# Kernel optimization log

Measured on AMD Instinct MI355X. Metric: run time of the kernel, lower is better.

## Reference

```python
import jax, jax.numpy as jnp
import numpy as np

D = 1024
H = 16
HD = D // H


def setup_inputs() -> dict:
    key = jax.random.key(0)
    ks = jax.random.split(key, 5)
    s = 1.0 / np.sqrt(D)
    return {
        "inputs": jax.random.normal(ks[0], (2, 2048, D), dtype=jnp.float32),
        "Wq": jax.random.normal(ks[1], (D, D), dtype=jnp.float32) * s,
        "bq": jnp.zeros((D,), jnp.float32),
        "Wk": jax.random.normal(ks[2], (D, D), dtype=jnp.float32) * s,
        "bk": jnp.zeros((D,), jnp.float32),
        "Wv": jax.random.normal(ks[3], (D, D), dtype=jnp.float32) * s,
        "bv": jnp.zeros((D,), jnp.float32),
        "Wo": jax.random.normal(ks[4], (D, D), dtype=jnp.float32) * s,
        "bo": jnp.zeros((D,), jnp.float32),
    }


def reference(inputs, Wq, bq, Wk, bk, Wv, bv, Wo, bo):
    B, S, _ = inputs.shape
    def split_heads(x):  # [B,S,D] -> [B,H,S,hd]
        return x.reshape(B, S, H, HD).transpose(0, 2, 1, 3)
    q = split_heads(inputs @ Wq + bq)
    k = split_heads(inputs @ Wk + bk)
    v = split_heads(inputs @ Wv + bv)
    scale = 1.0 / jnp.sqrt(jnp.asarray(HD, inputs.dtype))
    scores = jnp.einsum("bhsd,bhtd->bhst", q, k) * scale  # [B,H,S,S]
    weights = jax.nn.softmax(scores, axis=-1)
    attn = jnp.einsum("bhst,bhtd->bhsd", weights, v)
    concat = attn.transpose(0, 2, 1, 3).reshape(B, S, D)
    return concat @ Wo + bo
```

## Files before the change

### kernel.cpp

```cpp
#include <hip/hip_runtime.h>


typedef __bf16 bf16x8 __attribute__((ext_vector_type(8)));
typedef float  f32x4  __attribute__((ext_vector_type(4)));

#if __has_builtin(__builtin_amdgcn_exp2f)
#define EXPFN(x) __builtin_amdgcn_exp2f(x)
#define QSCALE (0.125f * 1.44269504088896f)
#else
#define EXPFN(x) __expf(x)
#define QSCALE 0.125f
#endif

#define LDKP 74

__device__ __forceinline__ unsigned short f2bf(float f) {
    unsigned int u = __float_as_uint(f);
    u += 0x7FFFu + ((u >> 16) & 1u);
    return (unsigned short)(u >> 16);
}

__device__ __forceinline__ void gload16(const void* g, void* l) {
    __builtin_amdgcn_global_load_lds(
        (const __attribute__((address_space(1))) void*)g,
        (__attribute__((address_space(3))) void*)l, 16, 0, 0);
}

#define WAIT0_BARRIER() asm volatile("s_waitcnt vmcnt(0)\n\ts_barrier" ::: "memory")

__global__ __launch_bounds__(256) void prep_kernel(
    const float* __restrict__ X, ushort4* __restrict__ Xb,
    const float* __restrict__ Wq, const float* __restrict__ Wk,
    const float* __restrict__ Wv, const float* __restrict__ Wo,
    unsigned short* __restrict__ Wt_all) {
    const int z = blockIdx.z;
    if (z == 4) {
        int base = (blockIdx.y * 32 + blockIdx.x) * 1024 + threadIdx.x;
        const float4* X4 = (const float4*)X;
        #pragma unroll
        for (int c = 0; c < 4; c++) {
            int i = base + c * 256;
            float4 v = X4[i];
            ushort4 o;
            o.x = f2bf(v.x); o.y = f2bf(v.y); o.z = f2bf(v.z); o.w = f2bf(v.w);
            Xb[i] = o;
        }
        return;
    }
    __shared__ float tile[32][33];
    const float* W = (z == 0) ? Wq : (z == 1) ? Wk : (z == 2) ? Wv : Wo;
    unsigned short* Wt = Wt_all + (size_t)z * 1024 * 1024;
    int c0 = blockIdx.x * 32, r0 = blockIdx.y * 32;
    int x = threadIdx.x & 31, y = threadIdx.x >> 5;
    for (int j = 0; j < 32; j += 8)
        tile[y + j][x] = W[(r0 + y + j) * 1024 + c0 + x];
    __syncthreads();
    for (int j = 0; j < 32; j += 8)
        Wt[(c0 + y + j) * 1024 + r0 + x] = f2bf(tile[x][y + j]);
}

__global__ __launch_bounds__(256) void gemm_qkv_kernel(
    const unsigned short* __restrict__ Xb, const unsigned short* __restrict__ Wt_all,
    const float* __restrict__ bq, const float* __restrict__ bk,
    const float* __restrict__ bv,
    unsigned short* __restrict__ Qb, unsigned short* __restrict__ Kb,
    unsigned short* __restrict__ Vt) {
    const int z = blockIdx.z;
    const int x0 = blockIdx.x * 128;
    const int y0 = blockIdx.y * 128;

    const unsigned short* Ap;
    const unsigned short* Bp;
    if (z < 2) {
        Ap = Xb + (size_t)x0 * 1024;
        Bp = Wt_all + (size_t)z * 1024 * 1024 + (size_t)y0 * 1024;
    } else {
        Ap = Wt_all + (size_t)2 * 1024 * 1024 + (size_t)y0 * 1024;
        Bp = Xb + (size_t)x0 * 1024;
    }

    __shared__ __align__(16) unsigned short As[128 * 64];
    __shared__ __align__(16) unsigned short Bs[128 * 64];

    const int tid = threadIdx.x;
    const int lane = tid & 63, wave = tid >> 6;
    const int quad = lane >> 4, l15 = lane & 15;
    const int wrow = (wave >> 1) * 64, wcol = (wave & 1) * 64;

    f32x4 acc[4][4] = {};

    const int srow = lane >> 3;
    const int ch8  = (lane & 7) * 8;
    const int swz  = (((lane & 7) ^ srow)) * 8;
    const int sw   = (l15 & 7);

    for (int k0 = 0; k0 < 1024; k0 += 64) {
        #pragma unroll
        for (int c = 0; c < 4; c++) {
            int r = c * 32 + wave * 8 + srow;
            gload16(Ap + (size_t)r * 1024 + k0 + swz, &As[r * 64 + ch8]);
            gload16(Bp + (size_t)r * 1024 + k0 + swz, &Bs[r * 64 + ch8]);
        }
        WAIT0_BARRIER();
        #pragma unroll
        for (int kk = 0; kk < 2; kk++) {
            bf16x8 af[4], bfr[4];
            #pragma unroll
            for (int i = 0; i < 4; i++)
                af[i] = *(const bf16x8*)&As[(wrow + i * 16 + l15) * 64 +
                                            (((kk * 4 + quad) ^ sw)) * 8];
            #pragma unroll
            for (int j = 0; j < 4; j++)
                bfr[j] = *(const bf16x8*)&Bs[(wcol + j * 16 + l15) * 64 +
                                             (((kk * 4 + quad) ^ sw)) * 8];
            #pragma unroll
            for (int i = 0; i < 4; i++)
                #pragma unroll
                for (int j = 0; j < 4; j++)
                    acc[i][j] = __builtin_amdgcn_mfma_f32_16x16x32_bf16(
                        af[i], bfr[j], acc[i][j], 0, 0, 0);
        }
        __syncthreads();
    }

    if (z < 2) {
        const float* bias = (z == 0) ? bq : bk;
        #pragma unroll
        for (int j = 0; j < 4; j++) {
            int col = y0 + wcol + j * 16 + l15;
            float bcol = bias[col];
            int h = col >> 6, d = col & 63;
            #pragma unroll
            for (int i = 0; i < 4; i++)
                #pragma unroll
                for (int r = 0; r < 4; r++) {
                    int row = x0 + wrow + i * 16 + quad * 4 + r;
                    int b = row >> 11, s = row & 2047;
                    float v = acc[i][j][r] + bcol;
                    if (z == 0)
                        Qb[(size_t)((b * 16 + h) * 2048 + s) * 64 + d] = f2bf(v * QSCALE);
                    else
                        Kb[(size_t)((b * 16 + h) * 2048 + s) * 64 + d] = f2bf(v);
                }
        }
    } else {
        #pragma unroll
        for (int i = 0; i < 4; i++)
            #pragma unroll
            for (int r = 0; r < 4; r++) {
                int rowd = y0 + wrow + i * 16 + quad * 4 + r;
                float brow = bv[rowd];
                #pragma unroll
                for (int j = 0; j < 4; j++) {
                    int colm = x0 + wcol + j * 16 + l15;
                    int b = colm >> 11, s = colm & 2047;
                    Vt[(size_t)(b * 1024 + rowd) * 2048 + s] = f2bf(acc[i][j][r] + brow);
                }
            }
    }
}

__global__ __launch_bounds__(256) void attn_kernel(
    const unsigned short* __restrict__ Qb, const unsigned short* __restrict__ Kb,
    const unsigned short* __restrict__ Vt, unsigned short* __restrict__ Cc,
    float* __restrict__ Op, float* __restrict__ Lp, int tlen, int do_split) {
    const int bh = blockIdx.y;
    const int b = bh >> 4, h = bh & 15;
    const int q0 = blockIdx.x * 128;
    const int split = blockIdx.z;
    const int tbeg = split * tlen;

    const int tid = threadIdx.x;
    const int lane = tid & 63, wave = tid >> 6;
    const int quad = lane >> 4, l15 = lane & 15;

    __shared__ __align__(16) unsigned short Ks[2][64 * 64];
    __shared__ __align__(16) unsigned short Vs[2][64 * 64];
    __shared__ __align__(16) unsigned short Ps[4][32 * LDKP];

    const unsigned short* Qbh = Qb + (size_t)bh * 2048 * 64;
    const unsigned short* Kbh = Kb + (size_t)bh * 2048 * 64;
    const unsigned short* Vbh = Vt + (size_t)bh * 64 * 2048;

    bf16x8 qa[2][2];
    #pragma unroll
    for (int mi = 0; mi < 2; mi++)
        #pragma unroll
        for (int kk = 0; kk < 2; kk++)
            qa[mi][kk] = *(const bf16x8*)&Qbh[
                (size_t)(q0 + wave * 32 + mi * 16 + l15) * 64 + kk * 32 + quad * 8];

    union { unsigned short us[8]; bf16x8 v; } ones_u;
    #pragma unroll
    for (int i = 0; i < 8; i++) ones_u.us[i] = 0x3F80;
    const bf16x8 onesv = ones_u.v;

    f32x4 o[2][4] = {};
    f32x4 ol[2] = {};

    const int srow = lane >> 3;
    const int r0s = wave * 16 + srow;
    const int ch8 = (lane & 7) * 8;
    const int swz = (((lane & 7) ^ srow)) * 8;
    const int sw  = (l15 & 7);

    {
        const int t0 = tbeg;
        gload16(&Kbh[(size_t)(t0 + r0s) * 64 + swz],       &Ks[0][r0s * 64 + ch8]);
        gload16(&Kbh[(size_t)(t0 + r0s + 8) * 64 + swz],   &Ks[0][(r0s + 8) * 64 + ch8]);
        gload16(&Vbh[(size_t)r0s * 2048 + t0 + swz],       &Vs[0][r0s * 64 + ch8]);
        gload16(&Vbh[(size_t)(r0s + 8) * 2048 + t0 + swz], &Vs[0][(r0s + 8) * 64 + ch8]);
    }

    const int niter = tlen >> 6;
    for (int it = 0; it < niter; it++) {
        const int cur = it & 1, nxt = cur ^ 1;
        WAIT0_BARRIER();
        if (it + 1 < niter) {
            const int t0 = tbeg + (it + 1) * 64;
            gload16(&Kbh[(size_t)(t0 + r0s) * 64 + swz],       &Ks[nxt][r0s * 64 + ch8]);
            gload16(&Kbh[(size_t)(t0 + r0s + 8) * 64 + swz],   &Ks[nxt][(r0s + 8) * 64 + ch8]);
            gload16(&Vbh[(size_t)r0s * 2048 + t0 + swz],       &Vs[nxt][r0s * 64 + ch8]);
            gload16(&Vbh[(size_t)(r0s + 8) * 2048 + t0 + swz], &Vs[nxt][(r0s + 8) * 64 + ch8]);
        }

        f32x4 sf[2][4] = {};
        #pragma unroll
        for (int j = 0; j < 4; j++)
            #pragma unroll
            for (int kk = 0; kk < 2; kk++) {
                bf16x8 kf = *(const bf16x8*)&Ks[cur][(j * 16 + l15) * 64 +
                                                     (((kk * 4 + quad) ^ sw)) * 8];
                sf[0][j] = __builtin_amdgcn_mfma_f32_16x16x32_bf16(qa[0][kk], kf, sf[0][j], 0, 0, 0);
                sf[1][j] = __builtin_amdgcn_mfma_f32_16x16x32_bf16(qa[1][kk], kf, sf[1][j], 0, 0, 0);
            }

        #pragma unroll
        for (int mi = 0; mi < 2; mi++)
            #pragma unroll
            for (int j = 0; j < 4; j++)
                #pragma unroll
                for (int r = 0; r < 4; r++) {
                    float p = EXPFN(sf[mi][j][r]);
                    Ps[wave][(mi * 16 + quad * 4 + r) * LDKP + j * 16 + l15] =
                        (unsigned short)(__float_as_uint(p) >> 16);
                }

        asm volatile("s_waitcnt lgkmcnt(0)" ::: "memory");

        #pragma unroll
        for (int kk = 0; kk < 2; kk++) {
            bf16x8 pf0 = *(const bf16x8*)&Ps[wave][(l15) * LDKP + kk * 32 + quad * 8];
            bf16x8 pf1 = *(const bf16x8*)&Ps[wave][(16 + l15) * LDKP + kk * 32 + quad * 8];
            ol[0] = __builtin_amdgcn_mfma_f32_16x16x32_bf16(pf0, onesv, ol[0], 0, 0, 0);
            ol[1] = __builtin_amdgcn_mfma_f32_16x16x32_bf16(pf1, onesv, ol[1], 0, 0, 0);
            #pragma unroll
            for (int j = 0; j < 4; j++) {
                bf16x8 vf = *(const bf16x8*)&Vs[cur][(j * 16 + l15) * 64 +
                                                     (((kk * 4 + quad) ^ sw)) * 8];
                o[0][j] = __builtin_amdgcn_mfma_f32_16x16x32_bf16(pf0, vf, o[0][j], 0, 0, 0);
                o[1][j] = __builtin_amdgcn_mfma_f32_16x16x32_bf16(pf1, vf, o[1][j], 0, 0, 0);
            }
        }
    }

    if (do_split) {
        float* Opd = Op + (size_t)(split * 32 + bh) * 2048 * 64;
        float* Lpd = Lp + (size_t)(split * 32 + bh) * 2048;
        #pragma unroll
        for (int mi = 0; mi < 2; mi++)
            #pragma unroll
            for (int r = 0; r < 4; r++) {
                int s = q0 + wave * 32 + mi * 16 + quad * 4 + r;
                if (l15 == 0) Lpd[s] = ol[mi][r];
                #pragma unroll
                for (int j = 0; j < 4; j++)
                    Opd[(size_t)s * 64 + j * 16 + l15] = o[mi][j][r];
            }
    } else {
        #pragma unroll
        for (int mi = 0; mi < 2; mi++)
            #pragma unroll
            for (int r = 0; r < 4; r++) {
                float inv = 1.f / ol[mi][r];
                int s = q0 + wave * 32 + mi * 16 + quad * 4 + r;
                size_t row = (size_t)(b * 2048 + s);
                #pragma unroll
                for (int j = 0; j < 4; j++)
                    Cc[row * 1024 + h * 64 + j * 16 + l15] = f2bf(o[mi][j][r] * inv);
            }
    }
}

__global__ __launch_bounds__(256) void combine_kernel(
    const float4* __restrict__ Op, const float* __restrict__ Lp,
    unsigned short* __restrict__ Cc) {
    int idx = blockIdx.x * 256 + threadIdx.x;
    int d4 = idx & 15;
    int s = (idx >> 4) & 2047;
    int bh = idx >> 15;
    const size_t half4 = (size_t)32 * 2048 * 16;
    float4 a = Op[(size_t)idx], c = Op[half4 + (size_t)idx];
    float l = Lp[bh * 2048 + s] + Lp[32 * 2048 + bh * 2048 + s];
    float inv = 1.f / l;
    ushort4 o;
    o.x = f2bf((a.x + c.x) * inv); o.y = f2bf((a.y + c.y) * inv);
    o.z = f2bf((a.z + c.z) * inv); o.w = f2bf((a.w + c.w) * inv);
    int b = bh >> 4, h = bh & 15;
    *(ushort4*)&Cc[((size_t)(b * 2048 + s)) * 1024 + h * 64 + d4 * 4] = o;
}

__global__ __launch_bounds__(256) void gemm_out_kernel(
    const unsigned short* __restrict__ Cc, const unsigned short* __restrict__ Wot,
    const float* __restrict__ bo, float* __restrict__ out) {
    const int m0 = blockIdx.x * 128;
    const int n0 = blockIdx.y * 64;

    __shared__ __align__(16) unsigned short As[128 * 64];
    __shared__ __align__(16) unsigned short Bs[64 * 64];

    const int tid = threadIdx.x;
    const int lane = tid & 63, wave = tid >> 6;
    const int quad = lane >> 4, l15 = lane & 15;
    const int wrow = (wave >> 1) * 64, wcol = (wave & 1) * 32;

    f32x4 acc[4][2] = {};
    const int srow = lane >> 3;
    const int ch8 = (lane & 7) * 8;
    const int swz = (((lane & 7) ^ srow)) * 8;
    const int sw  = (l15 & 7);

    for (int k0 = 0; k0 < 1024; k0 += 64) {
        #pragma unroll
        for (int c = 0; c < 4; c++) {
            int r = c * 32 + wave * 8 + srow;
            gload16(Cc + (size_t)(m0 + r) * 1024 + k0 + swz, &As[r * 64 + ch8]);
            if (c < 2)
                gload16(Wot + (size_t)(n0 + r) * 1024 + k0 + swz, &Bs[r * 64 + ch8]);
        }
        WAIT0_BARRIER();
        #pragma unroll
        for (int kk = 0; kk < 2; kk++) {
            bf16x8 af[4], bfr[2];
            #pragma unroll
            for (int i = 0; i < 4; i++)
                af[i] = *(const bf16x8*)&As[(wrow + i * 16 + l15) * 64 +
                                            (((kk * 4 + quad) ^ sw)) * 8];
            #pragma unroll
            for (int j = 0; j < 2; j++)
                bfr[j] = *(const bf16x8*)&Bs[(wcol + j * 16 + l15) * 64 +
                                             (((kk * 4 + quad) ^ sw)) * 8];
            #pragma unroll
            for (int i = 0; i < 4; i++)
                #pragma unroll
                for (int j = 0; j < 2; j++)
                    acc[i][j] = __builtin_amdgcn_mfma_f32_16x16x32_bf16(
                        af[i], bfr[j], acc[i][j], 0, 0, 0);
        }
        __syncthreads();
    }

    #pragma unroll
    for (int j = 0; j < 2; j++) {
        int col = n0 + wcol + j * 16 + l15;
        float bcol = bo[col];
        #pragma unroll
        for (int i = 0; i < 4; i++)
            #pragma unroll
            for (int r = 0; r < 4; r++) {
                int row = m0 + wrow + i * 16 + quad * 4 + r;
                out[(size_t)row * 1024 + col] = acc[i][j][r] + bcol;
            }
    }
}

extern "C" void kernel_launch(void* const* d_in, const int* in_sizes, int n_in,
                              void* d_out, int out_size, void* d_ws, size_t ws_size,
                              hipStream_t stream) {
    const float* X  = (const float*)d_in[0];
    const float* Wq = (const float*)d_in[1];
    const float* bq = (const float*)d_in[2];
    const float* Wk = (const float*)d_in[3];
    const float* bk = (const float*)d_in[4];
    const float* Wv = (const float*)d_in[5];
    const float* bv = (const float*)d_in[6];
    const float* Wo = (const float*)d_in[7];
    const float* bo = (const float*)d_in[8];
    float* out = (float*)d_out;

    char* ws = (char*)d_ws;
    unsigned short* Xb = (unsigned short*)(ws);
    unsigned short* Wt = (unsigned short*)(ws + (8u  << 20));
    unsigned short* Qb = (unsigned short*)(ws + (16u << 20));
    unsigned short* Kb = (unsigned short*)(ws + (24u << 20));
    unsigned short* Vt = (unsigned short*)(ws + (32u << 20));
    unsigned short* Cc = (unsigned short*)(ws + (40u << 20));
    float* Op = (float*)(ws + (48u << 20));
    float* Lp = (float*)(ws + (48u << 20) + 33554432u);
    const bool use_split = ws_size >= ((size_t)(48u << 20) + 33554432u + 524288u);

    prep_kernel<<<dim3(32, 32, 5), 256, 0, stream>>>(X, (ushort4*)Xb, Wq, Wk, Wv, Wo, Wt);
    gemm_qkv_kernel<<<dim3(32, 8, 3), 256, 0, stream>>>(Xb, Wt, bq, bk, bv, Qb, Kb, Vt);
    if (use_split) {
        attn_kernel<<<dim3(16, 32, 2), 256, 0, stream>>>(Qb, Kb, Vt, Cc, Op, Lp, 1024, 1);
        combine_kernel<<<4096, 256, 0, stream>>>((const float4*)Op, Lp, Cc);
    } else {
        attn_kernel<<<dim3(16, 32, 1), 256, 0, stream>>>(Qb, Kb, Vt, Cc, Op, Lp, 2048, 0);
    }
    gemm_out_kernel<<<dim3(32, 16), 256, 0, stream>>>(Cc, Wt + 3u * 1024 * 1024, bo, out);
}
```

Measured before the change: 208.3 us.

## Fuse Q and K projections sharing X tile; single-buffer attention K/V loads

The QKV GEMM now computes Q and K in one block, loading the X tile once and running two accumulator sets against separate Wq and Wk tiles. The grid shrinks from three z-slices to two, and launch bounds request two blocks per CU. Separately, the attention kernel drops its double-buffered K/V prefetch in favour of a single buffer that is loaded and waited on each iteration. This cuts LDS use but exposes global load latency. The doubled accumulators raise register pressure in the fused Q/K path.

```diff
diff --git a/kernel.cpp b/kernel.cpp
--- a/kernel.cpp
+++ b/kernel.cpp
@@ -59,7 +59,7 @@
         Wt[(c0 + y + j) * 1024 + r0 + x] = f2bf(tile[x][y + j]);
 }
 
-__global__ __launch_bounds__(256) void gemm_qkv_kernel(
+__global__ __launch_bounds__(256, 2) void gemm_qkv_kernel(
     const unsigned short* __restrict__ Xb, const unsigned short* __restrict__ Wt_all,
     const float* __restrict__ bq, const float* __restrict__ bk,
     const float* __restrict__ bv,
@@ -69,66 +69,68 @@
     const int x0 = blockIdx.x * 128;
     const int y0 = blockIdx.y * 128;
 
-    const unsigned short* Ap;
-    const unsigned short* Bp;
-    if (z < 2) {
-        Ap = Xb + (size_t)x0 * 1024;
-        Bp = Wt_all + (size_t)z * 1024 * 1024 + (size_t)y0 * 1024;
-    } else {
-        Ap = Wt_all + (size_t)2 * 1024 * 1024 + (size_t)y0 * 1024;
-        Bp = Xb + (size_t)x0 * 1024;
-    }
-
     __shared__ __align__(16) unsigned short As[128 * 64];
-    __shared__ __align__(16) unsigned short Bs[128 * 64];
+    __shared__ __align__(16) unsigned short Bs0[128 * 64];
+    __shared__ __align__(16) unsigned short Bs1[128 * 64];
 
     const int tid = threadIdx.x;
     const int lane = tid & 63, wave = tid >> 6;
     const int quad = lane >> 4, l15 = lane & 15;
     const int wrow = (wave >> 1) * 64, wcol = (wave & 1) * 64;
 
-    f32x4 acc[4][4] = {};
-
     const int srow = lane >> 3;
     const int ch8  = (lane & 7) * 8;
     const int swz  = (((lane & 7) ^ srow)) * 8;
     const int sw   = (l15 & 7);
 
-    for (int k0 = 0; k0 < 1024; k0 += 64) {
-        #pragma unroll
-        for (int c = 0; c < 4; c++) {
-            int r = c * 32 + wave * 8 + srow;
-            gload16(Ap + (size_t)r * 1024 + k0 + swz, &As[r * 64 + ch8]);
-            gload16(Bp + (size_t)r * 1024 + k0 + swz, &Bs[r * 64 + ch8]);
-        }
-        WAIT0_BARRIER();
-        #pragma unroll
-        for (int kk = 0; kk < 2; kk++) {
-            bf16x8 af[4], bfr[4];
-            #pragma unroll
-            for (int i = 0; i < 4; i++)
-                af[i] = *(const bf16x8*)&As[(wrow + i * 16 + l15) * 64 +
-                                            (((kk * 4 + quad) ^ sw)) * 8];
-            #pragma unroll
-            for (int j = 0; j < 4; j++)
-                bfr[j] = *(const bf16x8*)&Bs[(wcol + j * 16 + l15) * 64 +
-                                             (((kk * 4 + quad) ^ sw)) * 8];
-            #pragma unroll
-            for (int i = 0; i < 4; i++)
-                #pragma unroll
-                for (int j = 0; j < 4; j++)
-                    acc[i][j] = __builtin_amdgcn_mfma_f32_16x16x32_bf16(
-                        af[i], bfr[j], acc[i][j], 0, 0, 0);
-        }
-        __syncthreads();
-    }
-
-    if (z < 2) {
-        const float* bias = (z == 0) ? bq : bk;
+    if (z == 0) {
+        const unsigned short* Ap = Xb + (size_t)x0 * 1024;
+        const unsigned short* Bq = Wt_all + (size_t)y0 * 1024;
+        const unsigned short* Bk = Wt_all + (size_t)1024 * 1024 + (size_t)y0 * 1024;
+
+        f32x4 aq[4][4] = {};
+        f32x4 ak[4][4] = {};
+
+        for (int k0 = 0; k0 < 1024; k0 += 64) {
+            #pragma unroll
+            for (int c = 0; c < 4; c++) {
+                int r = c * 32 + wave * 8 + srow;
+                gload16(Ap + (size_t)r * 1024 + k0 + swz, &As[r * 64 + ch8]);
+                gload16(Bq + (size_t)r * 1024 + k0 + swz, &Bs0[r * 64 + ch8]);
+                gload16(Bk + (size_t)r * 1024 + k0 + swz, &Bs1[r * 64 + ch8]);
+            }
+            WAIT0_BARRIER();
+            #pragma unroll
+            for (int kk = 0; kk < 2; kk++) {
+                bf16x8 af[4], bqf[4], bkf[4];
+                #pragma unroll
+                for (int i = 0; i < 4; i++)
+                    af[i] = *(const bf16x8*)&As[(wrow + i * 16 + l15) * 64 +
+                                                (((kk * 4 + quad) ^ sw)) * 8];
+                #pragma unroll
+                for (int j = 0; j < 4; j++) {
+                    bqf[j] = *(const bf16x8*)&Bs0[(wcol + j * 16 + l15) * 64 +
+                                                  (((kk * 4 + quad) ^ sw)) * 8];
+                    bkf[j] = *(const bf16x8*)&Bs1[(wcol + j * 16 + l15) * 64 +
+                                                  (((kk * 4 + quad) ^ sw)) * 8];
+                }
+                #pragma unroll
+                for (int i = 0; i < 4; i++)
+                    #pragma unroll
+                    for (int j = 0; j < 4; j++) {
+                        aq[i][j] = __builtin_amdgcn_mfma_f32_16x16x32_bf16(
+                            af[i], bqf[j], aq[i][j], 0, 0, 0);
+                        ak[i][j] = __builtin_amdgcn_mfma_f32_16x16x32_bf16(
+                            af[i], bkf[j], ak[i][j], 0, 0, 0);
+                    }
+            }
+            __syncthreads();
+        }
+
         #pragma unroll
         for (int j = 0; j < 4; j++) {
             int col = y0 + wcol + j * 16 + l15;
-            float bcol = bias[col];
+            float bqc = bq[col], bkc = bk[col];
             int h = col >> 6, d = col & 63;
             #pragma unroll
             for (int i = 0; i < 4; i++)
@@ -136,14 +138,46 @@
                 for (int r = 0; r < 4; r++) {
                     int row = x0 + wrow + i * 16 + quad * 4 + r;
                     int b = row >> 11, s = row & 2047;
-                    float v = acc[i][j][r] + bcol;
-                    if (z == 0)
-                        Qb[(size_t)((b * 16 + h) * 2048 + s) * 64 + d] = f2bf(v * QSCALE);
-                    else
-                        Kb[(size_t)((b * 16 + h) * 2048 + s) * 64 + d] = f2bf(v);
+                    size_t idx = (size_t)((b * 16 + h) * 2048 + s) * 64 + d;
+                    Qb[idx] = f2bf((aq[i][j][r] + bqc) * QSCALE);
+                    Kb[idx] = f2bf(ak[i][j][r] + bkc);
                 }
         }
     } else {
+        const unsigned short* Ap = Wt_all + (size_t)2 * 1024 * 1024 + (size_t)y0 * 1024;
+        const unsigned short* Bp = Xb + (size_t)x0 * 1024;
+
+        f32x4 acc[4][4] = {};
+
+        for (int k0 = 0; k0 < 1024; k0 += 64) {
+            #pragma unroll
+            for (int c = 0; c < 4; c++) {
+                int r = c * 32 + wave * 8 + srow;
+                gload16(Ap + (size_t)r * 1024 + k0 + swz, &As[r * 64 + ch8]);
+                gload16(Bp + (size_t)r * 1024 + k0 + swz, &Bs0[r * 64 + ch8]);
+            }
+            WAIT0_BARRIER();
+            #pragma unroll
+            for (int kk = 0; kk < 2; kk++) {
+                bf16x8 af[4], bfr[4];
+                #pragma unroll
+                for (int i = 0; i < 4; i++)
+                    af[i] = *(const bf16x8*)&As[(wrow + i * 16 + l15) * 64 +
+                                                (((kk * 4 + quad) ^ sw)) * 8];
+                #pragma unroll
+                for (int j = 0; j < 4; j++)
+                    bfr[j] = *(const bf16x8*)&Bs0[(wcol + j * 16 + l15) * 64 +
+                                                  (((kk * 4 + quad) ^ sw)) * 8];
+                #pragma unroll
+                for (int i = 0; i < 4; i++)
+                    #pragma unroll
+                    for (int j = 0; j < 4; j++)
+                        acc[i][j] = __builtin_amdgcn_mfma_f32_16x16x32_bf16(
+                            af[i], bfr[j], acc[i][j], 0, 0, 0);
+            }
+            __syncthreads();
+        }
+
         #pragma unroll
         for (int i = 0; i < 4; i++)
             #pragma unroll
@@ -174,8 +208,8 @@
     const int lane = tid & 63, wave = tid >> 6;
     const int quad = lane >> 4, l15 = lane & 15;
 
-    __shared__ __align__(16) unsigned short Ks[2][64 * 64];
-    __shared__ __align__(16) unsigned short Vs[2][64 * 64];
+    __shared__ __align__(16) unsigned short Ks[64 * 64];
+    __shared__ __align__(16) unsigned short Vs[64 * 64];
     __shared__ __align__(16) unsigned short Ps[4][32 * LDKP];
 
     const unsigned short* Qbh = Qb + (size_t)bh * 2048 * 64;
@@ -204,33 +238,23 @@
     const int swz = (((lane & 7) ^ srow)) * 8;
     const int sw  = (l15 & 7);
 
-    {
-        const int t0 = tbeg;
-        gload16(&Kbh[(size_t)(t0 + r0s) * 64 + swz],       &Ks[0][r0s * 64 + ch8]);
-        gload16(&Kbh[(size_t)(t0 + r0s + 8) * 64 + swz],   &Ks[0][(r0s + 8) * 64 + ch8]);
-        gload16(&Vbh[(size_t)r0s * 2048 + t0 + swz],       &Vs[0][r0s * 64 + ch8]);
-        gload16(&Vbh[(size_t)(r0s + 8) * 2048 + t0 + swz], &Vs[0][(r0s + 8) * 64 + ch8]);
-    }
-
-    const int niter = tlen >> 6;
-    for (int it = 0; it < niter; it++) {
-        const int cur = it & 1, nxt = cur ^ 1;
-        WAIT0_BARRIER();
-        if (it + 1 < niter) {
-            const int t0 = tbeg + (it + 1) * 64;
-            gload16(&Kbh[(size_t)(t0 + r0s) * 64 + swz],       &Ks[nxt][r0s * 64 + ch8]);
-            gload16(&Kbh[(size_t)(t0 + r0s + 8) * 64 + swz],   &Ks[nxt][(r0s + 8) * 64 + ch8]);
-            gload16(&Vbh[(size_t)r0s * 2048 + t0 + swz],       &Vs[nxt][r0s * 64 + ch8]);
-            gload16(&Vbh[(size_t)(r0s + 8) * 2048 + t0 + swz], &Vs[nxt][(r0s + 8) * 64 + ch8]);
-        }
+    for (int ti = 0; ti < tlen; ti += 64) {
+        const int t0 = tbeg + ti;
+        __syncthreads();
+        gload16(&Kbh[(size_t)(t0 + r0s) * 64 + swz],       &Ks[r0s * 64 + ch8]);
+        gload16(&Kbh[(size_t)(t0 + r0s + 8) * 64 + swz],   &Ks[(r0s + 8) * 64 + ch8]);
+        gload16(&Vbh[(size_t)r0s * 2048 + t0 + swz],       &Vs[r0s * 64 + ch8]);
+        gload16(&Vbh[(size_t)(r0s + 8) * 2048 + t0 + swz], &Vs[(r0s + 8) * 64 + ch8]);
+        asm volatile("s_waitcnt vmcnt(0)" ::: "memory");
+        __syncthreads();
 
         f32x4 sf[2][4] = {};
         #pragma unroll
         for (int j = 0; j < 4; j++)
             #pragma unroll
             for (int kk = 0; kk < 2; kk++) {
-                bf16x8 kf = *(const bf16x8*)&Ks[cur][(j * 16 + l15) * 64 +
-                                                     (((kk * 4 + quad) ^ sw)) * 8];
+                bf16x8 kf = *(const bf16x8*)&Ks[(j * 16 + l15) * 64 +
+                                                (((kk * 4 + quad) ^ sw)) * 8];
                 sf[0][j] = __builtin_amdgcn_mfma_f32_16x16x32_bf16(qa[0][kk], kf, sf[0][j], 0, 0, 0);
                 sf[1][j] = __builtin_amdgcn_mfma_f32_16x16x32_bf16(qa[1][kk], kf, sf[1][j], 0, 0, 0);
             }
@@ -256,8 +280,8 @@
             ol[1] = __builtin_amdgcn_mfma_f32_16x16x32_bf16(pf1, onesv, ol[1], 0, 0, 0);
             #pragma unroll
             for (int j = 0; j < 4; j++) {
-                bf16x8 vf = *(const bf16x8*)&Vs[cur][(j * 16 + l15) * 64 +
-                                                     (((kk * 4 + quad) ^ sw)) * 8];
+                bf16x8 vf = *(const bf16x8*)&Vs[(j * 16 + l15) * 64 +
+                                                (((kk * 4 + quad) ^ sw)) * 8];
                 o[0][j] = __builtin_amdgcn_mfma_f32_16x16x32_bf16(pf0, vf, o[0][j], 0, 0, 0);
                 o[1][j] = __builtin_amdgcn_mfma_f32_16x16x32_bf16(pf1, vf, o[1][j], 0, 0, 0);
             }
@@ -400,7 +424,7 @@
     const bool use_split = ws_size >= ((size_t)(48u << 20) + 33554432u + 524288u);
 
     prep_kernel<<<dim3(32, 32, 5), 256, 0, stream>>>(X, (ushort4*)Xb, Wq, Wk, Wv, Wo, Wt);
-    gemm_qkv_kernel<<<dim3(32, 8, 3), 256, 0, stream>>>(Xb, Wt, bq, bk, bv, Qb, Kb, Vt);
+    gemm_qkv_kernel<<<dim3(32, 8, 2), 256, 0, stream>>>(Xb, Wt, bq, bk, bv, Qb, Kb, Vt);
     if (use_split) {
         attn_kernel<<<dim3(16, 32, 2), 256, 0, stream>>>(Qb, Kb, Vt, Cc, Op, Lp, 1024, 1);
         combine_kernel<<<4096, 256, 0, stream>>>((const float4*)Op, Lp, Cc);
```

Measured after the change: 195.0 us. -6.4%, faster.
